# Performance work log

Measured on AMD Instinct MI355X. Metric: run time of the kernel, lower is better.

The kernel has to match this reference:

```python
import jax, jax.numpy as jnp
import numpy as np

N = 20000        # nodes
E = 320000       # edges (avg degree 16)
NHID = 256       # hidden dim (decoder input features)
NFEAT = 256      # reconstructed attribute dim
K_SELECTED = 4096  # number of nodes with label == 1 (static for jit)


def setup_inputs() -> dict:
    key = jax.random.key(0)
    ks = jax.random.split(key, 12)
    feature_attribute = jax.random.normal(ks[0], (N, NHID), dtype=jnp.float32)
    edge_row = jax.random.randint(ks[1], (E,), 0, N, dtype=jnp.int32)
    edge_col = jax.random.randint(ks[2], (E,), 0, N, dtype=jnp.int32)
    # positive, roughly degree-normalized adjacency weights
    edge_w = jax.random.uniform(ks[3], (E,), dtype=jnp.float32) / 16.0
    # first K_SELECTED nodes are labeled 1, rest 0 (static count for jit)
    labels = jnp.concatenate([jnp.ones((K_SELECTED,), jnp.int32),
                              jnp.zeros((N - K_SELECTED,), jnp.int32)])
    stdv1 = 1.0 / np.sqrt(NHID)
    stdv2 = 1.0 / np.sqrt(NFEAT)
    W1_ad = jax.random.uniform(ks[4], (NHID, NHID), minval=-stdv1, maxval=stdv1, dtype=jnp.float32)
    b1_ad = jax.random.uniform(ks[5], (NHID,), minval=-stdv1, maxval=stdv1, dtype=jnp.float32)
    W2_ad = jax.random.uniform(ks[6], (NHID, NFEAT), minval=-stdv2, maxval=stdv2, dtype=jnp.float32)
    b2_ad = jax.random.uniform(ks[7], (NFEAT,), minval=-stdv2, maxval=stdv2, dtype=jnp.float32)
    W_sd = jax.random.uniform(ks[8], (NHID, NHID), minval=-stdv1, maxval=stdv1, dtype=jnp.float32)
    b_sd = jax.random.uniform(ks[9], (NHID,), minval=-stdv1, maxval=stdv1, dtype=jnp.float32)
    return dict(feature_attribute=feature_attribute, edge_row=edge_row, edge_col=edge_col,
                edge_w=edge_w, labels=labels, W1_ad=W1_ad, b1_ad=b1_ad,
                W2_ad=W2_ad, b2_ad=b2_ad, W_sd=W_sd, b_sd=b_sd)


def reference(feature_attribute, edge_row, edge_col, edge_w, labels,
              W1_ad, b1_ad, W2_ad, b2_ad, W_sd, b_sd):
    def gcn(x, W, b):
        support = x @ W                                   # [N, d_out] dense mm
        msg = support[edge_col] * edge_w[:, None]         # gather + scale [E, d_out]
        out = jax.ops.segment_sum(msg, edge_row, num_segments=N)  # spmm aggregation
        return out + b

    # static-size index of labeled nodes (labels==1 count is K_SELECTED)
    idx = jnp.nonzero(labels == 1, size=K_SELECTED)[0]

    # Attribute decoder: relu(gc1) -> (dropout, eval: identity) -> gc2 -> select
    h = jax.nn.relu(gcn(feature_attribute, W1_ad, b1_ad))
    pred_attribute_mat = gcn(h, W2_ad, b2_ad)[idx]        # [K, NFEAT]

    # Structure decoder: gc1 -> select -> x @ x.T
    s = gcn(feature_attribute, W_sd, b_sd)[idx]           # [K, NHID]
    pred_adj_mat = s @ s.T                                # [K, K]

    return pred_attribute_mat, pred_adj_mat
```

## Files before the change

kernel.cpp:

```cpp
#include <hip/hip_runtime.h>
#include <hip/hip_bf16.h>

#define NN   20000
#define NE   320000
#define KSEL 4096

typedef short bf16x8 __attribute__((ext_vector_type(8)));
typedef float f32x4  __attribute__((ext_vector_type(4)));

static __device__ __forceinline__ float bf2f(unsigned short u){
  return __uint_as_float(((unsigned int)u) << 16);
}
static __device__ __forceinline__ unsigned short f2bf(float f){
  unsigned int x = __float_as_uint(f);
  x += 0x7fffu + ((x >> 16) & 1u);
  return (unsigned short)(x >> 16);
}
static __device__ __forceinline__ void gld_lds16(const unsigned short* g, unsigned short* l){
  __builtin_amdgcn_global_load_lds(
      (const __attribute__((address_space(1))) unsigned int*)g,
      (__attribute__((address_space(3))) unsigned int*)l, 16, 0, 0);
}

__global__ void k_cvt_x(const float* __restrict__ X, unsigned short* __restrict__ Xb){
  int i = (blockIdx.x * 256 + threadIdx.x) * 4;
  float4 v = *(const float4*)(X + i);
  ushort4 o = { f2bf(v.x), f2bf(v.y), f2bf(v.z), f2bf(v.w) };
  *(ushort4*)(Xb + i) = o;
}

__global__ void k_cvt_w(const float* __restrict__ W1, const float* __restrict__ Wsd,
                        const float* __restrict__ W2, unsigned short* __restrict__ Wt){
  int t = blockIdx.x * 256 + threadIdx.x;
  int w = t >> 16;
  int o = (t >> 8) & 255;
  int k = t & 255;
  const float* W = (w == 0) ? W1 : (w == 1 ? Wsd : W2);
  Wt[t] = f2bf(W[k * 256 + o]);
}

__global__ __launch_bounds__(256) void k_scan_part(const int* __restrict__ v, int n, int isLabel,
                                                   int* __restrict__ part){
  __shared__ int ws[4];
  int tid = threadIdx.x, lane = tid & 63, wv = tid >> 6;
  int base = blockIdx.x * 1024 + tid * 4;
  int s = 0;
  #pragma unroll
  for (int j = 0; j < 4; ++j){
    int n0 = base + j;
    if (n0 < n) s += isLabel ? (v[n0] == 1 ? 1 : 0) : v[n0];
  }
  #pragma unroll
  for (int off = 32; off; off >>= 1) s += __shfl_down(s, off, 64);
  if (lane == 0) ws[wv] = s;
  __syncthreads();
  if (tid == 0) part[blockIdx.x] = ws[0] + ws[1] + ws[2] + ws[3];
}

__global__ __launch_bounds__(64) void k_scan_offs(int* __restrict__ part, int P){
  int lane = threadIdx.x;
  int v = (lane < P) ? part[lane] : 0;
  int acc = v;
  #pragma unroll
  for (int off = 1; off < 64; off <<= 1){
    int t = __shfl_up(acc, off, 64);
    if (lane >= off) acc += t;
  }
  if (lane < P) part[lane] = acc - v;
}

__global__ __launch_bounds__(256) void k_idx_emit(const int* __restrict__ labels,
    const int* __restrict__ part, int* __restrict__ idx){
  __shared__ int ws[4];
  int tid = threadIdx.x, lane = tid & 63, wv = tid >> 6;
  int base = blockIdx.x * 1024 + tid * 4;
  int c[4]; int s = 0;
  #pragma unroll
  for (int j = 0; j < 4; ++j){
    int n0 = base + j;
    c[j] = (n0 < NN && labels[n0] == 1) ? 1 : 0;
    s += c[j];
  }
  int incl = s;
  #pragma unroll
  for (int off = 1; off < 64; off <<= 1){
    int t = __shfl_up(incl, off, 64);
    if (lane >= off) incl += t;
  }
  if (lane == 63) ws[wv] = incl;
  __syncthreads();
  int woff = part[blockIdx.x];
  for (int w = 0; w < wv; ++w) woff += ws[w];
  int off = woff + incl - s;
  #pragma unroll
  for (int j = 0; j < 4; ++j){
    if (c[j]){ if (off < KSEL) idx[off] = base + j; ++off; }
  }
}

__global__ __launch_bounds__(256) void k_row_emit(const int* __restrict__ counts,
    const int* __restrict__ part, int* __restrict__ start, int* __restrict__ cursor){
  __shared__ int ws[4];
  int tid = threadIdx.x, lane = tid & 63, wv = tid >> 6;
  int base = blockIdx.x * 1024 + tid * 4;
  int c[4]; int s = 0;
  #pragma unroll
  for (int j = 0; j < 4; ++j){
    int n0 = base + j;
    c[j] = (n0 < NN) ? counts[n0] : 0;
    s += c[j];
  }
  int incl = s;
  #pragma unroll
  for (int off = 1; off < 64; off <<= 1){
    int t = __shfl_up(incl, off, 64);
    if (lane >= off) incl += t;
  }
  if (lane == 63) ws[wv] = incl;
  __syncthreads();
  int woff = part[blockIdx.x];
  for (int w = 0; w < wv; ++w) woff += ws[w];
  int run = woff + incl - s;
  #pragma unroll
  for (int j = 0; j < 4; ++j){
    int n0 = base + j;
    if (n0 < NN){ start[n0] = run; cursor[n0] = run; run += c[j]; }
  }
  if (blockIdx.x == 0 && tid == 0) start[NN] = NE;
}

__global__ void k_hist(const int* __restrict__ row, int* __restrict__ counts){
  int e = blockIdx.x * 256 + threadIdx.x;
  if (e < NE) atomicAdd(&counts[row[e]], 1);
}

__global__ void k_scatter(const int* __restrict__ row, const int* __restrict__ col,
                          const float* __restrict__ ew, int* __restrict__ cursor,
                          int2* __restrict__ rec){
  int e = blockIdx.x * 256 + threadIdx.x;
  if (e < NE){
    int r = row[e];
    int p = atomicAdd(&cursor[r], 1);
    rec[p] = make_int2(col[e], __float_as_int(ew[e]));
  }
}

__global__ __launch_bounds__(256) void k_gemm(const unsigned short* __restrict__ A,
                                              const unsigned short* __restrict__ Wt,
                                              unsigned short* __restrict__ out,
                                              int M, int ldo){
  __shared__ unsigned short At[128 * 64];
  __shared__ unsigned short Bt[64 * 64];
  int tid = threadIdx.x, wave = tid >> 6, lane = tid & 63;
  int lm = lane & 15, lq = lane >> 4;
  int mBase = blockIdx.x * 128;
  int oBase = blockIdx.y * 64;
  f32x4 acc[2][4] = {};
  for (int kc = 0; kc < 256; kc += 64){
    if (kc) __syncthreads();
    #pragma unroll
    for (int it = 0; it < 4; ++it){
      int s = (wave * 4 + it) * 64 + lane;
      int row = s >> 3, c = (s & 7) ^ (row & 7);
      int gr = mBase + row; if (gr >= M) gr = M - 1;
      gld_lds16(&A[(size_t)gr * 256 + kc + c * 8], &At[s * 8]);
    }
    #pragma unroll
    for (int it = 0; it < 2; ++it){
      int s = (wave * 2 + it) * 64 + lane;
      int row = s >> 3, c = (s & 7) ^ (row & 7);
      gld_lds16(&Wt[(size_t)(oBase + row) * 256 + kc + c * 8], &Bt[s * 8]);
    }
    __syncthreads();
    #pragma unroll
    for (int ks = 0; ks < 64; ks += 32){
      int cb = ks >> 3;
      int RA = wave * 32 + lm;
      int ca = ((cb + lq) ^ (RA & 7)) << 3;
      bf16x8 a0 = *(const bf16x8*)&At[RA * 64 + ca];
      bf16x8 a1 = *(const bf16x8*)&At[(RA + 16) * 64 + ca];
      #pragma unroll
      for (int os = 0; os < 4; ++os){
        int RB = os * 16 + lm;
        bf16x8 b = *(const bf16x8*)&Bt[RB * 64 + (((cb + lq) ^ (RB & 7)) << 3)];
        acc[0][os] = __builtin_amdgcn_mfma_f32_16x16x32_bf16(a0, b, acc[0][os], 0, 0, 0);
        acc[1][os] = __builtin_amdgcn_mfma_f32_16x16x32_bf16(a1, b, acc[1][os], 0, 0, 0);
      }
    }
  }
  #pragma unroll
  for (int ms = 0; ms < 2; ++ms){
    int rb = mBase + wave * 32 + ms * 16 + lq * 4;
    #pragma unroll
    for (int os = 0; os < 4; ++os){
      int col = oBase + os * 16 + lm;
      #pragma unroll
      for (int r = 0; r < 4; ++r){
        int row = rb + r;
        if (row < M) out[(size_t)row * ldo + col] = f2bf(acc[ms][os][r]);
      }
    }
  }
}

__global__ __launch_bounds__(256) void k_gemm_out(const unsigned short* __restrict__ A,
                                                  const unsigned short* __restrict__ Wt2,
                                                  const float* __restrict__ bias,
                                                  float* __restrict__ out){
  __shared__ unsigned short lds[64 * 264];
  int tid = threadIdx.x;
  int wave = tid >> 6, lane = tid & 63;
  int lm = lane & 15, lq = lane >> 4;
  int mBase = blockIdx.x * 128;
  int oBase = blockIdx.y * 64;
  #pragma unroll
  for (int it = 0; it < 8; ++it){
    int c = it * 256 + tid;
    int o = c >> 5, kk = (c & 31) << 3;
    *(bf16x8*)&lds[o * 264 + kk] = *(const bf16x8*)&Wt2[(oBase + o) * 256 + kk];
  }
  __syncthreads();
  f32x4 acc[2][4] = {};
  int r0 = mBase + wave * 32 + lm;
  #pragma unroll
  for (int ks = 0; ks < 256; ks += 32){
    int ka = ks + lq * 8;
    bf16x8 a0 = *(const bf16x8*)&A[(size_t)r0 * 256 + ka];
    bf16x8 a1 = *(const bf16x8*)&A[(size_t)(r0 + 16) * 256 + ka];
    #pragma unroll
    for (int os = 0; os < 4; ++os){
      bf16x8 b = *(const bf16x8*)&lds[(os * 16 + lm) * 264 + ka];
      acc[0][os] = __builtin_amdgcn_mfma_f32_16x16x32_bf16(a0, b, acc[0][os], 0, 0, 0);
      acc[1][os] = __builtin_amdgcn_mfma_f32_16x16x32_bf16(a1, b, acc[1][os], 0, 0, 0);
    }
  }
  #pragma unroll
  for (int ms = 0; ms < 2; ++ms){
    int rb = mBase + wave * 32 + ms * 16 + lq * 4;
    #pragma unroll
    for (int os = 0; os < 4; ++os){
      int col = oBase + os * 16 + lm;
      float bv = bias[col];
      #pragma unroll
      for (int r = 0; r < 4; ++r)
        out[(size_t)(rb + r) * 256 + col] = acc[ms][os][r] + bv;
    }
  }
}

__global__ __launch_bounds__(256) void k_gemm_st(const unsigned short* __restrict__ S,
                                                 float* __restrict__ out1){
  __shared__ unsigned short At[128 * 64];
  __shared__ unsigned short Bt[128 * 64];
  int tid = threadIdx.x, wave = tid >> 6, lane = tid & 63;
  int lm = lane & 15, lq = lane >> 4;
  int mBase = blockIdx.x * 128;
  int oBase = blockIdx.y * 128;
  f32x4 acc[2][8] = {};
  for (int kc = 0; kc < 256; kc += 64){
    if (kc) __syncthreads();
    #pragma unroll
    for (int it = 0; it < 4; ++it){
      int s = (wave * 4 + it) * 64 + lane;
      int row = s >> 3, c = (s & 7) ^ (row & 7);
      gld_lds16(&S[(size_t)(mBase + row) * 256 + kc + c * 8], &At[s * 8]);
      gld_lds16(&S[(size_t)(oBase + row) * 256 + kc + c * 8], &Bt[s * 8]);
    }
    __syncthreads();
    #pragma unroll
    for (int ks = 0; ks < 64; ks += 32){
      int cb = ks >> 3;
      int RA = wave * 32 + lm;
      int ca = ((cb + lq) ^ (RA & 7)) << 3;
      bf16x8 a0 = *(const bf16x8*)&At[RA * 64 + ca];
      bf16x8 a1 = *(const bf16x8*)&At[(RA + 16) * 64 + ca];
      #pragma unroll
      for (int os = 0; os < 8; ++os){
        int RB = os * 16 + lm;
        bf16x8 b = *(const bf16x8*)&Bt[RB * 64 + (((cb + lq) ^ (RB & 7)) << 3)];
        acc[0][os] = __builtin_amdgcn_mfma_f32_16x16x32_bf16(a0, b, acc[0][os], 0, 0, 0);
        acc[1][os] = __builtin_amdgcn_mfma_f32_16x16x32_bf16(a1, b, acc[1][os], 0, 0, 0);
      }
    }
  }
  #pragma unroll
  for (int ms = 0; ms < 2; ++ms){
    int rb = mBase + wave * 32 + ms * 16 + lq * 4;
    #pragma unroll
    for (int os = 0; os < 8; ++os){
      int col = oBase + os * 16 + lm;
      #pragma unroll
      for (int r = 0; r < 4; ++r)
        out1[(size_t)(rb + r) * 4096 + col] = acc[ms][os][r];
    }
  }
}

__global__ __launch_bounds__(256) void k_spmm1(const unsigned short* __restrict__ supX,
    const int* __restrict__ start, const int2* __restrict__ rec,
    const float* __restrict__ b1, unsigned short* __restrict__ h){
  int wave = threadIdx.x >> 6, lane = threadIdx.x & 63;
  int n = blockIdx.x * 4 + wave;
  int s = start[n], e = start[n + 1];
  int d = lane * 4;
  float a0 = 0, a1 = 0, a2 = 0, a3 = 0;
  for (int base = s; base < e; base += 64){
    int p = base + lane;
    int pc = p < e ? p : e - 1;
    int2 r = rec[pc];
    float wv = (p < e) ? __int_as_float(r.y) : 0.0f;
    int m = e - base; if (m > 64) m = 64;
    for (int j = 0; j < m; j += 4){
      int   c0 = __shfl(r.x, j),     c1 = __shfl(r.x, j + 1);
      int   c2 = __shfl(r.x, j + 2), c3 = __shfl(r.x, j + 3);
      float w0 = __shfl(wv, j),      w1 = __shfl(wv, j + 1);
      float w2 = __shfl(wv, j + 2),  w3 = __shfl(wv, j + 3);
      ushort4 v0 = *(const ushort4*)&supX[(size_t)c0 * 512 + d];
      ushort4 v1 = *(const ushort4*)&supX[(size_t)c1 * 512 + d];
      ushort4 v2 = *(const ushort4*)&supX[(size_t)c2 * 512 + d];
      ushort4 v3 = *(const ushort4*)&supX[(size_t)c3 * 512 + d];
      a0 += w0 * bf2f(v0.x) + w1 * bf2f(v1.x) + w2 * bf2f(v2.x) + w3 * bf2f(v3.x);
      a1 += w0 * bf2f(v0.y) + w1 * bf2f(v1.y) + w2 * bf2f(v2.y) + w3 * bf2f(v3.y);
      a2 += w0 * bf2f(v0.z) + w1 * bf2f(v1.z) + w2 * bf2f(v2.z) + w3 * bf2f(v3.z);
      a3 += w0 * bf2f(v0.w) + w1 * bf2f(v1.w) + w2 * bf2f(v2.w) + w3 * bf2f(v3.w);
    }
  }
  float4 b = *(const float4*)&b1[d];
  ushort4 o = { f2bf(fmaxf(a0 + b.x, 0.f)), f2bf(fmaxf(a1 + b.y, 0.f)),
                f2bf(fmaxf(a2 + b.z, 0.f)), f2bf(fmaxf(a3 + b.w, 0.f)) };
  *(ushort4*)&h[(size_t)n * 256 + d] = o;
}

__global__ __launch_bounds__(256) void k_spmm_sel(const unsigned short* __restrict__ supX,
    const unsigned short* __restrict__ h, const int* __restrict__ idx,
    const int* __restrict__ start, const int2* __restrict__ rec,
    const float* __restrict__ bsd,
    unsigned short* __restrict__ aggH, unsigned short* __restrict__ sel){
  int wave = threadIdx.x >> 6, lane = threadIdx.x & 63;
  int i = blockIdx.x * 4 + wave;
  int n = idx[i];
  int s = start[n], e = start[n + 1];
  int d = lane * 4;
  float h0 = 0, h1 = 0, h2 = 0, h3 = 0;
  float s0 = 0, s1 = 0, s2 = 0, s3 = 0;
  for (int base = s; base < e; base += 64){
    int p = base + lane;
    int pc = p < e ? p : e - 1;
    int2 r = rec[pc];
    float wv = (p < e) ? __int_as_float(r.y) : 0.0f;
    int m = e - base; if (m > 64) m = 64;
    for (int j = 0; j < m; j += 2){
      int   c0 = __shfl(r.x, j), c1 = __shfl(r.x, j + 1);
      float w0 = __shfl(wv, j),  w1 = __shfl(wv, j + 1);
      ushort4 hv0 = *(const ushort4*)&h[(size_t)c0 * 256 + d];
      ushort4 sv0 = *(const ushort4*)&supX[(size_t)c0 * 512 + 256 + d];
      ushort4 hv1 = *(const ushort4*)&h[(size_t)c1 * 256 + d];
      ushort4 sv1 = *(const ushort4*)&supX[(size_t)c1 * 512 + 256 + d];
      h0 += w0 * bf2f(hv0.x) + w1 * bf2f(hv1.x);
      h1 += w0 * bf2f(hv0.y) + w1 * bf2f(hv1.y);
      h2 += w0 * bf2f(hv0.z) + w1 * bf2f(hv1.z);
      h3 += w0 * bf2f(hv0.w) + w1 * bf2f(hv1.w);
      s0 += w0 * bf2f(sv0.x) + w1 * bf2f(sv1.x);
      s1 += w0 * bf2f(sv0.y) + w1 * bf2f(sv1.y);
      s2 += w0 * bf2f(sv0.z) + w1 * bf2f(sv1.z);
      s3 += w0 * bf2f(sv0.w) + w1 * bf2f(sv1.w);
    }
  }
  ushort4 oh = { f2bf(h0), f2bf(h1), f2bf(h2), f2bf(h3) };
  *(ushort4*)&aggH[(size_t)i * 256 + d] = oh;
  float4 b = *(const float4*)&bsd[d];
  ushort4 os_ = { f2bf(s0 + b.x), f2bf(s1 + b.y), f2bf(s2 + b.z), f2bf(s3 + b.w) };
  *(ushort4*)&sel[(size_t)i * 256 + d] = os_;
}

extern "C" void kernel_launch(void* const* d_in, const int* in_sizes, int n_in,
                              void* d_out, int out_size, void* d_ws, size_t ws_size,
                              hipStream_t stream){
  const float* X    = (const float*)d_in[0];
  const int*   erow = (const int*)d_in[1];
  const int*   ecol = (const int*)d_in[2];
  const float* ew   = (const float*)d_in[3];
  const int*   labels = (const int*)d_in[4];
  const float* W1   = (const float*)d_in[5];
  const float* b1   = (const float*)d_in[6];
  const float* W2   = (const float*)d_in[7];
  const float* b2   = (const float*)d_in[8];
  const float* Wsd  = (const float*)d_in[9];
  const float* bsd  = (const float*)d_in[10];
  float* out0 = (float*)d_out;
  float* out1 = out0 + (size_t)KSEL * 256;

  char* ws = (char*)d_ws;
  unsigned short* Xb   = (unsigned short*)(ws);
  unsigned short* Wt   = (unsigned short*)(ws + 10240000);
  unsigned short* supX = (unsigned short*)(ws + 10633216);
  unsigned short* h    = (unsigned short*)(ws + 31113216);
  unsigned short* aggH = (unsigned short*)(ws + 41353216);
  unsigned short* sel  = (unsigned short*)(ws + 43450368);
  int* idx    = (int*)(ws + 45547520);
  int* counts = (int*)(ws + 45563904);
  int* startp = (int*)(ws + 45643904);
  int* cursor = (int*)(ws + 45723908);
  int2* rec   = (int2*)(ws + 45803912);
  int* partA  = (int*)(ws + 48363912);
  int* partB  = (int*)(ws + 48364040);

  hipMemsetAsync(counts, 0, NN * sizeof(int), stream);
  k_cvt_x<<<5000, 256, 0, stream>>>(X, Xb);
  k_cvt_w<<<768, 256, 0, stream>>>(W1, Wsd, W2, Wt);
  k_scan_part<<<20, 256, 0, stream>>>(labels, NN, 1, partA);
  k_scan_offs<<<1, 64, 0, stream>>>(partA, 20);
  k_idx_emit<<<20, 256, 0, stream>>>(labels, partA, idx);
  k_hist<<<NE / 256, 256, 0, stream>>>(erow, counts);
  k_scan_part<<<20, 256, 0, stream>>>(counts, NN, 0, partB);
  k_scan_offs<<<1, 64, 0, stream>>>(partB, 20);
  k_row_emit<<<20, 256, 0, stream>>>(counts, partB, startp, cursor);
  k_scatter<<<NE / 256, 256, 0, stream>>>(erow, ecol, ew, cursor, rec);
  k_gemm<<<dim3(157, 8), 256, 0, stream>>>(Xb, Wt, supX, NN, 512);
  k_spmm1<<<5000, 256, 0, stream>>>(supX, startp, rec, b1, h);
  k_spmm_sel<<<1024, 256, 0, stream>>>(supX, h, idx, startp, rec, bsd, aggH, sel);
  k_gemm_out<<<dim3(32, 4), 256, 0, stream>>>(aggH, Wt + 512 * 256, b2, out0);
  k_gemm_st<<<dim3(32, 32), 256, 0, stream>>>(sel, out1);
}
```

Measured before the change: 224.7 us.

## Aggregate before projecting and fuse prep kernels to cut GEMM and launches

Uses associativity (A·X)·W = A·(X·W) to run the sparse aggregation once on the raw features, shared by both first-layer GCNs. The full first-layer GEMM now covers only the W1 projection, and the structure decoder projects just the selected rows. The conversion, count-zeroing and label partial sums are merged into one prep kernel, and the separate scan-offset kernels are folded into the emit kernels, which removes several launches and the memset. The catch is that the row-emit blocks each re-sum the prefix of counts redundantly, and bf16 rounding now happens at a different point than before.

```diff
diff --git a/kernel.cpp b/kernel.cpp
--- a/kernel.cpp
+++ b/kernel.cpp
@@ -22,57 +22,61 @@
       (__attribute__((address_space(3))) unsigned int*)l, 16, 0, 0);
 }
 
-__global__ void k_cvt_x(const float* __restrict__ X, unsigned short* __restrict__ Xb){
-  int i = (blockIdx.x * 256 + threadIdx.x) * 4;
-  float4 v = *(const float4*)(X + i);
-  ushort4 o = { f2bf(v.x), f2bf(v.y), f2bf(v.z), f2bf(v.w) };
-  *(ushort4*)(Xb + i) = o;
-}
-
-__global__ void k_cvt_w(const float* __restrict__ W1, const float* __restrict__ Wsd,
-                        const float* __restrict__ W2, unsigned short* __restrict__ Wt){
-  int t = blockIdx.x * 256 + threadIdx.x;
-  int w = t >> 16;
-  int o = (t >> 8) & 255;
-  int k = t & 255;
-  const float* W = (w == 0) ? W1 : (w == 1 ? Wsd : W2);
-  Wt[t] = f2bf(W[k * 256 + o]);
-}
-
-__global__ __launch_bounds__(256) void k_scan_part(const int* __restrict__ v, int n, int isLabel,
-                                                   int* __restrict__ part){
+__global__ __launch_bounds__(256) void k_prep(const float* __restrict__ X,
+    const float* __restrict__ W1, const float* __restrict__ Wsd, const float* __restrict__ W2,
+    const int* __restrict__ labels,
+    unsigned short* __restrict__ Xb, unsigned short* __restrict__ Wt,
+    int* __restrict__ counts, int* __restrict__ partA){
+  int b = blockIdx.x, tid = threadIdx.x;
+  if (b < 5000){
+    int i = (b * 256 + tid) * 4;
+    float4 v = *(const float4*)(X + i);
+    ushort4 o = { f2bf(v.x), f2bf(v.y), f2bf(v.z), f2bf(v.w) };
+    *(ushort4*)(Xb + i) = o;
+  } else if (b < 5768){
+    int t = (b - 5000) * 256 + tid;
+    int w = t >> 16, o = (t >> 8) & 255, k = t & 255;
+    const float* W = (w == 0) ? W1 : (w == 1 ? Wsd : W2);
+    Wt[t] = f2bf(W[k * 256 + o]);
+  } else {
+    __shared__ int ws[4];
+    int z = b - 5768, lane = tid & 63, wv = tid >> 6;
+    if (tid < 250) *(int4*)&counts[z * 1000 + tid * 4] = make_int4(0, 0, 0, 0);
+    int base = z * 1024 + tid * 4;
+    int s = 0;
+    #pragma unroll
+    for (int j = 0; j < 4; ++j){
+      int n0 = base + j;
+      if (n0 < NN) s += (labels[n0] == 1) ? 1 : 0;
+    }
+    #pragma unroll
+    for (int off = 32; off; off >>= 1) s += __shfl_down(s, off, 64);
+    if (lane == 0) ws[wv] = s;
+    __syncthreads();
+    if (tid == 0) partA[z] = ws[0] + ws[1] + ws[2] + ws[3];
+  }
+}
+
+__global__ void k_hist(const int* __restrict__ row, int* __restrict__ counts){
+  int e = blockIdx.x * 256 + threadIdx.x;
+  if (e < NE) atomicAdd(&counts[row[e]], 1);
+}
+
+__global__ __launch_bounds__(256) void k_idx_emit(const int* __restrict__ labels,
+    const int* __restrict__ partA, int* __restrict__ idx){
   __shared__ int ws[4];
+  __shared__ int boff_s;
   int tid = threadIdx.x, lane = tid & 63, wv = tid >> 6;
-  int base = blockIdx.x * 1024 + tid * 4;
-  int s = 0;
-  #pragma unroll
-  for (int j = 0; j < 4; ++j){
-    int n0 = base + j;
-    if (n0 < n) s += isLabel ? (v[n0] == 1 ? 1 : 0) : v[n0];
-  }
-  #pragma unroll
-  for (int off = 32; off; off >>= 1) s += __shfl_down(s, off, 64);
-  if (lane == 0) ws[wv] = s;
-  __syncthreads();
-  if (tid == 0) part[blockIdx.x] = ws[0] + ws[1] + ws[2] + ws[3];
-}
-
-__global__ __launch_bounds__(64) void k_scan_offs(int* __restrict__ part, int P){
-  int lane = threadIdx.x;
-  int v = (lane < P) ? part[lane] : 0;
-  int acc = v;
-  #pragma unroll
-  for (int off = 1; off < 64; off <<= 1){
-    int t = __shfl_up(acc, off, 64);
-    if (lane >= off) acc += t;
-  }
-  if (lane < P) part[lane] = acc - v;
-}
-
-__global__ __launch_bounds__(256) void k_idx_emit(const int* __restrict__ labels,
-    const int* __restrict__ part, int* __restrict__ idx){
-  __shared__ int ws[4];
-  int tid = threadIdx.x, lane = tid & 63, wv = tid >> 6;
+  if (tid < 64){
+    int v = (lane < 20) ? partA[lane] : 0;
+    int acc = v;
+    #pragma unroll
+    for (int off = 1; off < 32; off <<= 1){
+      int t = __shfl_up(acc, off, 64);
+      if (lane >= off) acc += t;
+    }
+    if (lane == (int)blockIdx.x) boff_s = acc - v;
+  }
   int base = blockIdx.x * 1024 + tid * 4;
   int c[4]; int s = 0;
   #pragma unroll
@@ -89,7 +93,7 @@
   }
   if (lane == 63) ws[wv] = incl;
   __syncthreads();
-  int woff = part[blockIdx.x];
+  int woff = boff_s;
   for (int w = 0; w < wv; ++w) woff += ws[w];
   int off = woff + incl - s;
   #pragma unroll
@@ -99,14 +103,26 @@
 }
 
 __global__ __launch_bounds__(256) void k_row_emit(const int* __restrict__ counts,
-    const int* __restrict__ part, int* __restrict__ start, int* __restrict__ cursor){
+    int* __restrict__ start, int* __restrict__ cursor){
   __shared__ int ws[4];
+  __shared__ int red[4];
   int tid = threadIdx.x, lane = tid & 63, wv = tid >> 6;
-  int base = blockIdx.x * 1024 + tid * 4;
+  int base = blockIdx.x * 1024;
+  int ps = 0;
+  for (int i = tid * 4; i < base; i += 1024){
+    int4 v = *(const int4*)&counts[i];
+    ps += v.x + v.y + v.z + v.w;
+  }
+  #pragma unroll
+  for (int off = 32; off; off >>= 1) ps += __shfl_down(ps, off, 64);
+  if (lane == 0) red[wv] = ps;
+  __syncthreads();
+  int bpref = red[0] + red[1] + red[2] + red[3];
+  int nb = base + tid * 4;
   int c[4]; int s = 0;
   #pragma unroll
   for (int j = 0; j < 4; ++j){
-    int n0 = base + j;
+    int n0 = nb + j;
     c[j] = (n0 < NN) ? counts[n0] : 0;
     s += c[j];
   }
@@ -118,20 +134,15 @@
   }
   if (lane == 63) ws[wv] = incl;
   __syncthreads();
-  int woff = part[blockIdx.x];
+  int woff = bpref;
   for (int w = 0; w < wv; ++w) woff += ws[w];
   int run = woff + incl - s;
   #pragma unroll
   for (int j = 0; j < 4; ++j){
-    int n0 = base + j;
+    int n0 = nb + j;
     if (n0 < NN){ start[n0] = run; cursor[n0] = run; run += c[j]; }
   }
   if (blockIdx.x == 0 && tid == 0) start[NN] = NE;
-}
-
-__global__ void k_hist(const int* __restrict__ row, int* __restrict__ counts){
-  int e = blockIdx.x * 256 + threadIdx.x;
-  if (e < NE) atomicAdd(&counts[row[e]], 1);
 }
 
 __global__ void k_scatter(const int* __restrict__ row, const int* __restrict__ col,
@@ -145,160 +156,9 @@
   }
 }
 
-__global__ __launch_bounds__(256) void k_gemm(const unsigned short* __restrict__ A,
-                                              const unsigned short* __restrict__ Wt,
-                                              unsigned short* __restrict__ out,
-                                              int M, int ldo){
-  __shared__ unsigned short At[128 * 64];
-  __shared__ unsigned short Bt[64 * 64];
-  int tid = threadIdx.x, wave = tid >> 6, lane = tid & 63;
-  int lm = lane & 15, lq = lane >> 4;
-  int mBase = blockIdx.x * 128;
-  int oBase = blockIdx.y * 64;
-  f32x4 acc[2][4] = {};
-  for (int kc = 0; kc < 256; kc += 64){
-    if (kc) __syncthreads();
-    #pragma unroll
-    for (int it = 0; it < 4; ++it){
-      int s = (wave * 4 + it) * 64 + lane;
-      int row = s >> 3, c = (s & 7) ^ (row & 7);
-      int gr = mBase + row; if (gr >= M) gr = M - 1;
-      gld_lds16(&A[(size_t)gr * 256 + kc + c * 8], &At[s * 8]);
-    }
-    #pragma unroll
-    for (int it = 0; it < 2; ++it){
-      int s = (wave * 2 + it) * 64 + lane;
-      int row = s >> 3, c = (s & 7) ^ (row & 7);
-      gld_lds16(&Wt[(size_t)(oBase + row) * 256 + kc + c * 8], &Bt[s * 8]);
-    }
-    __syncthreads();
-    #pragma unroll
-    for (int ks = 0; ks < 64; ks += 32){
-      int cb = ks >> 3;
-      int RA = wave * 32 + lm;
-      int ca = ((cb + lq) ^ (RA & 7)) << 3;
-      bf16x8 a0 = *(const bf16x8*)&At[RA * 64 + ca];
-      bf16x8 a1 = *(const bf16x8*)&At[(RA + 16) * 64 + ca];
-      #pragma unroll
-      for (int os = 0; os < 4; ++os){
-        int RB = os * 16 + lm;
-        bf16x8 b = *(const bf16x8*)&Bt[RB * 64 + (((cb + lq) ^ (RB & 7)) << 3)];
-        acc[0][os] = __builtin_amdgcn_mfma_f32_16x16x32_bf16(a0, b, acc[0][os], 0, 0, 0);
-        acc[1][os] = __builtin_amdgcn_mfma_f32_16x16x32_bf16(a1, b, acc[1][os], 0, 0, 0);
-      }
-    }
-  }
-  #pragma unroll
-  for (int ms = 0; ms < 2; ++ms){
-    int rb = mBase + wave * 32 + ms * 16 + lq * 4;
-    #pragma unroll
-    for (int os = 0; os < 4; ++os){
-      int col = oBase + os * 16 + lm;
-      #pragma unroll
-      for (int r = 0; r < 4; ++r){
-        int row = rb + r;
-        if (row < M) out[(size_t)row * ldo + col] = f2bf(acc[ms][os][r]);
-      }
-    }
-  }
-}
-
-__global__ __launch_bounds__(256) void k_gemm_out(const unsigned short* __restrict__ A,
-                                                  const unsigned short* __restrict__ Wt2,
-                                                  const float* __restrict__ bias,
-                                                  float* __restrict__ out){
-  __shared__ unsigned short lds[64 * 264];
-  int tid = threadIdx.x;
-  int wave = tid >> 6, lane = tid & 63;
-  int lm = lane & 15, lq = lane >> 4;
-  int mBase = blockIdx.x * 128;
-  int oBase = blockIdx.y * 64;
-  #pragma unroll
-  for (int it = 0; it < 8; ++it){
-    int c = it * 256 + tid;
-    int o = c >> 5, kk = (c & 31) << 3;
-    *(bf16x8*)&lds[o * 264 + kk] = *(const bf16x8*)&Wt2[(oBase + o) * 256 + kk];
-  }
-  __syncthreads();
-  f32x4 acc[2][4] = {};
-  int r0 = mBase + wave * 32 + lm;
-  #pragma unroll
-  for (int ks = 0; ks < 256; ks += 32){
-    int ka = ks + lq * 8;
-    bf16x8 a0 = *(const bf16x8*)&A[(size_t)r0 * 256 + ka];
-    bf16x8 a1 = *(const bf16x8*)&A[(size_t)(r0 + 16) * 256 + ka];
-    #pragma unroll
-    for (int os = 0; os < 4; ++os){
-      bf16x8 b = *(const bf16x8*)&lds[(os * 16 + lm) * 264 + ka];
-      acc[0][os] = __builtin_amdgcn_mfma_f32_16x16x32_bf16(a0, b, acc[0][os], 0, 0, 0);
-      acc[1][os] = __builtin_amdgcn_mfma_f32_16x16x32_bf16(a1, b, acc[1][os], 0, 0, 0);
-    }
-  }
-  #pragma unroll
-  for (int ms = 0; ms < 2; ++ms){
-    int rb = mBase + wave * 32 + ms * 16 + lq * 4;
-    #pragma unroll
-    for (int os = 0; os < 4; ++os){
-      int col = oBase + os * 16 + lm;
-      float bv = bias[col];
-      #pragma unroll
-      for (int r = 0; r < 4; ++r)
-        out[(size_t)(rb + r) * 256 + col] = acc[ms][os][r] + bv;
-    }
-  }
-}
-
-__global__ __launch_bounds__(256) void k_gemm_st(const unsigned short* __restrict__ S,
-                                                 float* __restrict__ out1){
-  __shared__ unsigned short At[128 * 64];
-  __shared__ unsigned short Bt[128 * 64];
-  int tid = threadIdx.x, wave = tid >> 6, lane = tid & 63;
-  int lm = lane & 15, lq = lane >> 4;
-  int mBase = blockIdx.x * 128;
-  int oBase = blockIdx.y * 128;
-  f32x4 acc[2][8] = {};
-  for (int kc = 0; kc < 256; kc += 64){
-    if (kc) __syncthreads();
-    #pragma unroll
-    for (int it = 0; it < 4; ++it){
-      int s = (wave * 4 + it) * 64 + lane;
-      int row = s >> 3, c = (s & 7) ^ (row & 7);
-      gld_lds16(&S[(size_t)(mBase + row) * 256 + kc + c * 8], &At[s * 8]);
-      gld_lds16(&S[(size_t)(oBase + row) * 256 + kc + c * 8], &Bt[s * 8]);
-    }
-    __syncthreads();
-    #pragma unroll
-    for (int ks = 0; ks < 64; ks += 32){
-      int cb = ks >> 3;
-      int RA = wave * 32 + lm;
-      int ca = ((cb + lq) ^ (RA & 7)) << 3;
-      bf16x8 a0 = *(const bf16x8*)&At[RA * 64 + ca];
-      bf16x8 a1 = *(const bf16x8*)&At[(RA + 16) * 64 + ca];
-      #pragma unroll
-      for (int os = 0; os < 8; ++os){
-        int RB = os * 16 + lm;
-        bf16x8 b = *(const bf16x8*)&Bt[RB * 64 + (((cb + lq) ^ (RB & 7)) << 3)];
-        acc[0][os] = __builtin_amdgcn_mfma_f32_16x16x32_bf16(a0, b, acc[0][os], 0, 0, 0);
-        acc[1][os] = __builtin_amdgcn_mfma_f32_16x16x32_bf16(a1, b, acc[1][os], 0, 0, 0);
-      }
-    }
-  }
-  #pragma unroll
-  for (int ms = 0; ms < 2; ++ms){
-    int rb = mBase + wave * 32 + ms * 16 + lq * 4;
-    #pragma unroll
-    for (int os = 0; os < 8; ++os){
-      int col = oBase + os * 16 + lm;
-      #pragma unroll
-      for (int r = 0; r < 4; ++r)
-        out1[(size_t)(rb + r) * 4096 + col] = acc[ms][os][r];
-    }
-  }
-}
-
-__global__ __launch_bounds__(256) void k_spmm1(const unsigned short* __restrict__ supX,
+__global__ __launch_bounds__(256) void k_spmm_full(const unsigned short* __restrict__ Xb,
     const int* __restrict__ start, const int2* __restrict__ rec,
-    const float* __restrict__ b1, unsigned short* __restrict__ h){
+    unsigned short* __restrict__ aggX){
   int wave = threadIdx.x >> 6, lane = threadIdx.x & 63;
   int n = blockIdx.x * 4 + wave;
   int s = start[n], e = start[n + 1];
@@ -315,62 +175,220 @@
       int   c2 = __shfl(r.x, j + 2), c3 = __shfl(r.x, j + 3);
       float w0 = __shfl(wv, j),      w1 = __shfl(wv, j + 1);
       float w2 = __shfl(wv, j + 2),  w3 = __shfl(wv, j + 3);
-      ushort4 v0 = *(const ushort4*)&supX[(size_t)c0 * 512 + d];
-      ushort4 v1 = *(const ushort4*)&supX[(size_t)c1 * 512 + d];
-      ushort4 v2 = *(const ushort4*)&supX[(size_t)c2 * 512 + d];
-      ushort4 v3 = *(const ushort4*)&supX[(size_t)c3 * 512 + d];
+      ushort4 v0 = *(const ushort4*)&Xb[(size_t)c0 * 256 + d];
+      ushort4 v1 = *(const ushort4*)&Xb[(size_t)c1 * 256 + d];
+      ushort4 v2 = *(const ushort4*)&Xb[(size_t)c2 * 256 + d];
+      ushort4 v3 = *(const ushort4*)&Xb[(size_t)c3 * 256 + d];
       a0 += w0 * bf2f(v0.x) + w1 * bf2f(v1.x) + w2 * bf2f(v2.x) + w3 * bf2f(v3.x);
       a1 += w0 * bf2f(v0.y) + w1 * bf2f(v1.y) + w2 * bf2f(v2.y) + w3 * bf2f(v3.y);
       a2 += w0 * bf2f(v0.z) + w1 * bf2f(v1.z) + w2 * bf2f(v2.z) + w3 * bf2f(v3.z);
       a3 += w0 * bf2f(v0.w) + w1 * bf2f(v1.w) + w2 * bf2f(v2.w) + w3 * bf2f(v3.w);
     }
   }
-  float4 b = *(const float4*)&b1[d];
-  ushort4 o = { f2bf(fmaxf(a0 + b.x, 0.f)), f2bf(fmaxf(a1 + b.y, 0.f)),
-                f2bf(fmaxf(a2 + b.z, 0.f)), f2bf(fmaxf(a3 + b.w, 0.f)) };
-  *(ushort4*)&h[(size_t)n * 256 + d] = o;
-}
-
-__global__ __launch_bounds__(256) void k_spmm_sel(const unsigned short* __restrict__ supX,
-    const unsigned short* __restrict__ h, const int* __restrict__ idx,
-    const int* __restrict__ start, const int2* __restrict__ rec,
-    const float* __restrict__ bsd,
-    unsigned short* __restrict__ aggH, unsigned short* __restrict__ sel){
+  ushort4 o = { f2bf(a0), f2bf(a1), f2bf(a2), f2bf(a3) };
+  *(ushort4*)&aggX[(size_t)n * 256 + d] = o;
+}
+
+__global__ __launch_bounds__(256) void k_gemm_h(const unsigned short* __restrict__ A,
+                                                const unsigned short* __restrict__ Wt,
+                                                const float* __restrict__ bias,
+                                                unsigned short* __restrict__ out, int M){
+  __shared__ unsigned short At[128 * 64];
+  __shared__ unsigned short Bt[64 * 64];
+  int tid = threadIdx.x, wave = tid >> 6, lane = tid & 63;
+  int lm = lane & 15, lq = lane >> 4;
+  int mBase = blockIdx.x * 128;
+  int oBase = blockIdx.y * 64;
+  f32x4 acc[2][4] = {};
+  for (int kc = 0; kc < 256; kc += 64){
+    if (kc) __syncthreads();
+    #pragma unroll
+    for (int it = 0; it < 4; ++it){
+      int s = (wave * 4 + it) * 64 + lane;
+      int row = s >> 3, c = (s & 7) ^ (row & 7);
+      int gr = mBase + row; if (gr >= M) gr = M - 1;
+      gld_lds16(&A[(size_t)gr * 256 + kc + c * 8], &At[s * 8]);
+    }
+    #pragma unroll
+    for (int it = 0; it < 2; ++it){
+      int s = (wave * 2 + it) * 64 + lane;
+      int row = s >> 3, c = (s & 7) ^ (row & 7);
+      gld_lds16(&Wt[(size_t)(oBase + row) * 256 + kc + c * 8], &Bt[s * 8]);
+    }
+    __syncthreads();
+    #pragma unroll
+    for (int ks = 0; ks < 64; ks += 32){
+      int cb = ks >> 3;
+      int RA = wave * 32 + lm;
+      int ca = ((cb + lq) ^ (RA & 7)) << 3;
+      bf16x8 a0 = *(const bf16x8*)&At[RA * 64 + ca];
+      bf16x8 a1 = *(const bf16x8*)&At[(RA + 16) * 64 + ca];
+      #pragma unroll
+      for (int os = 0; os < 4; ++os){
+        int RB = os * 16 + lm;
+        bf16x8 b = *(const bf16x8*)&Bt[RB * 64 + (((cb + lq) ^ (RB & 7)) << 3)];
+        acc[0][os] = __builtin_amdgcn_mfma_f32_16x16x32_bf16(a0, b, acc[0][os], 0, 0, 0);
+        acc[1][os] = __builtin_amdgcn_mfma_f32_16x16x32_bf16(a1, b, acc[1][os], 0, 0, 0);
+      }
+    }
+  }
+  #pragma unroll
+  for (int ms = 0; ms < 2; ++ms){
+    int rb = mBase + wave * 32 + ms * 16 + lq * 4;
+    #pragma unroll
+    for (int os = 0; os < 4; ++os){
+      int col = oBase + os * 16 + lm;
+      float bv = bias[col];
+      #pragma unroll
+      for (int r = 0; r < 4; ++r){
+        int row = rb + r;
+        if (row < M) out[(size_t)row * 256 + col] = f2bf(fmaxf(acc[ms][os][r] + bv, 0.f));
+      }
+    }
+  }
+}
+
+__global__ __launch_bounds__(256) void k_spmm_selH(const unsigned short* __restrict__ h,
+    const int* __restrict__ idx, const int* __restrict__ start, const int2* __restrict__ rec,
+    unsigned short* __restrict__ aggH){
   int wave = threadIdx.x >> 6, lane = threadIdx.x & 63;
   int i = blockIdx.x * 4 + wave;
   int n = idx[i];
   int s = start[n], e = start[n + 1];
   int d = lane * 4;
-  float h0 = 0, h1 = 0, h2 = 0, h3 = 0;
-  float s0 = 0, s1 = 0, s2 = 0, s3 = 0;
+  float a0 = 0, a1 = 0, a2 = 0, a3 = 0;
   for (int base = s; base < e; base += 64){
     int p = base + lane;
     int pc = p < e ? p : e - 1;
     int2 r = rec[pc];
     float wv = (p < e) ? __int_as_float(r.y) : 0.0f;
     int m = e - base; if (m > 64) m = 64;
-    for (int j = 0; j < m; j += 2){
-      int   c0 = __shfl(r.x, j), c1 = __shfl(r.x, j + 1);
-      float w0 = __shfl(wv, j),  w1 = __shfl(wv, j + 1);
-      ushort4 hv0 = *(const ushort4*)&h[(size_t)c0 * 256 + d];
-      ushort4 sv0 = *(const ushort4*)&supX[(size_t)c0 * 512 + 256 + d];
-      ushort4 hv1 = *(const ushort4*)&h[(size_t)c1 * 256 + d];
-      ushort4 sv1 = *(const ushort4*)&supX[(size_t)c1 * 512 + 256 + d];
-      h0 += w0 * bf2f(hv0.x) + w1 * bf2f(hv1.x);
-      h1 += w0 * bf2f(hv0.y) + w1 * bf2f(hv1.y);
-      h2 += w0 * bf2f(hv0.z) + w1 * bf2f(hv1.z);
-      h3 += w0 * bf2f(hv0.w) + w1 * bf2f(hv1.w);
-      s0 += w0 * bf2f(sv0.x) + w1 * bf2f(sv1.x);
-      s1 += w0 * bf2f(sv0.y) + w1 * bf2f(sv1.y);
-      s2 += w0 * bf2f(sv0.z) + w1 * bf2f(sv1.z);
-      s3 += w0 * bf2f(sv0.w) + w1 * bf2f(sv1.w);
-    }
-  }
-  ushort4 oh = { f2bf(h0), f2bf(h1), f2bf(h2), f2bf(h3) };
-  *(ushort4*)&aggH[(size_t)i * 256 + d] = oh;
-  float4 b = *(const float4*)&bsd[d];
-  ushort4 os_ = { f2bf(s0 + b.x), f2bf(s1 + b.y), f2bf(s2 + b.z), f2bf(s3 + b.w) };
-  *(ushort4*)&sel[(size_t)i * 256 + d] = os_;
+    for (int j = 0; j < m; j += 4){
+      int   c0 = __shfl(r.x, j),     c1 = __shfl(r.x, j + 1);
+      int   c2 = __shfl(r.x, j + 2), c3 = __shfl(r.x, j + 3);
+      float w0 = __shfl(wv, j),      w1 = __shfl(wv, j + 1);
+      float w2 = __shfl(wv, j + 2),  w3 = __shfl(wv, j + 3);
+      ushort4 v0 = *(const ushort4*)&h[(size_t)c0 * 256 + d];
+      ushort4 v1 = *(const ushort4*)&h[(size_t)c1 * 256 + d];
+      ushort4 v2 = *(const ushort4*)&h[(size_t)c2 * 256 + d];
+      ushort4 v3 = *(const ushort4*)&h[(size_t)c3 * 256 + d];
+      a0 += w0 * bf2f(v0.x) + w1 * bf2f(v1.x) + w2 * bf2f(v2.x) + w3 * bf2f(v3.x);
+      a1 += w0 * bf2f(v0.y) + w1 * bf2f(v1.y) + w2 * bf2f(v2.y) + w3 * bf2f(v3.y);
+      a2 += w0 * bf2f(v0.z) + w1 * bf2f(v1.z) + w2 * bf2f(v2.z) + w3 * bf2f(v3.z);
+      a3 += w0 * bf2f(v0.w) + w1 * bf2f(v1.w) + w2 * bf2f(v2.w) + w3 * bf2f(v3.w);
+    }
+  }
+  ushort4 o = { f2bf(a0), f2bf(a1), f2bf(a2), f2bf(a3) };
+  *(ushort4*)&aggH[(size_t)i * 256 + d] = o;
+}
+
+__global__ __launch_bounds__(256) void k_gemm_os(const unsigned short* __restrict__ aggH,
+    const unsigned short* __restrict__ aggX, const int* __restrict__ idx,
+    const unsigned short* __restrict__ Wt,
+    const float* __restrict__ b2, const float* __restrict__ bsd,
+    float* __restrict__ out0, unsigned short* __restrict__ sel){
+  __shared__ unsigned short lds[64 * 264];
+  int tid = threadIdx.x;
+  int wave = tid >> 6, lane = tid & 63;
+  int lm = lane & 15, lq = lane >> 4;
+  int z = blockIdx.z;
+  int mBase = blockIdx.x * 128;
+  int oBase = blockIdx.y * 64;
+  const unsigned short* Wt2 = Wt + (z ? 256 * 256 : 512 * 256);
+  const float* bias = z ? bsd : b2;
+  #pragma unroll
+  for (int it = 0; it < 8; ++it){
+    int c = it * 256 + tid;
+    int o = c >> 5, kk = (c & 31) << 3;
+    *(bf16x8*)&lds[o * 264 + kk] = *(const bf16x8*)&Wt2[(oBase + o) * 256 + kk];
+  }
+  __syncthreads();
+  int r0 = mBase + wave * 32 + lm;
+  const unsigned short* A0;
+  const unsigned short* A1;
+  if (z){
+    A0 = aggX + (size_t)idx[r0] * 256;
+    A1 = aggX + (size_t)idx[r0 + 16] * 256;
+  } else {
+    A0 = aggH + (size_t)r0 * 256;
+    A1 = aggH + (size_t)(r0 + 16) * 256;
+  }
+  f32x4 acc[2][4] = {};
+  #pragma unroll
+  for (int ks = 0; ks < 256; ks += 32){
+    int ka = ks + lq * 8;
+    bf16x8 a0 = *(const bf16x8*)&A0[ka];
+    bf16x8 a1 = *(const bf16x8*)&A1[ka];
+    #pragma unroll
+    for (int os = 0; os < 4; ++os){
+      bf16x8 b = *(const bf16x8*)&lds[(os * 16 + lm) * 264 + ka];
+      acc[0][os] = __builtin_amdgcn_mfma_f32_16x16x32_bf16(a0, b, acc[0][os], 0, 0, 0);
+      acc[1][os] = __builtin_amdgcn_mfma_f32_16x16x32_bf16(a1, b, acc[1][os], 0, 0, 0);
+    }
+  }
+  #pragma unroll
+  for (int ms = 0; ms < 2; ++ms){
+    int rb = mBase + wave * 32 + ms * 16 + lq * 4;
+    #pragma unroll
+    for (int os = 0; os < 4; ++os){
+      int col = oBase + os * 16 + lm;
+      float bv = bias[col];
+      #pragma unroll
+      for (int r = 0; r < 4; ++r){
+        float v = acc[ms][os][r] + bv;
+        if (z) sel[(size_t)(rb + r) * 256 + col] = f2bf(v);
+        else   out0[(size_t)(rb + r) * 256 + col] = v;
+      }
+    }
+  }
+}
+
+__global__ __launch_bounds__(256) void k_gemm_st(const unsigned short* __restrict__ S,
+                                                 float* __restrict__ out1){
+  __shared__ unsigned short At[128 * 64];
+  __shared__ unsigned short Bt[128 * 64];
+  int tid = threadIdx.x, wave = tid >> 6, lane = tid & 63;
+  int lm = lane & 15, lq = lane >> 4;
+  int mBase = blockIdx.x * 128;
+  int oBase = blockIdx.y * 128;
+  f32x4 acc[2][8] = {};
+  for (int kc = 0; kc < 256; kc += 64){
+    if (kc) __syncthreads();
+    #pragma unroll
+    for (int it = 0; it < 4; ++it){
+      int s = (wave * 4 + it) * 64 + lane;
+      int row = s >> 3, c = (s & 7) ^ (row & 7);
+      gld_lds16(&S[(size_t)(mBase + row) * 256 + kc + c * 8], &At[s * 8]);
+      gld_lds16(&S[(size_t)(oBase + row) * 256 + kc + c * 8], &Bt[s * 8]);
+    }
+    __syncthreads();
+    #pragma unroll
+    for (int ks = 0; ks < 64; ks += 32){
+      int cb = ks >> 3;
+      int RA = wave * 32 + lm;
+      int ca = ((cb + lq) ^ (RA & 7)) << 3;
+      bf16x8 a0 = *(const bf16x8*)&At[RA * 64 + ca];
+      bf16x8 a1 = *(const bf16x8*)&At[(RA + 16) * 64 + ca];
+      #pragma unroll
+      for (int os = 0; os < 8; ++os){
+        int RB = os * 16 + lm;
+        bf16x8 b = *(const bf16x8*)&Bt[RB * 64 + (((cb + lq) ^ (RB & 7)) << 3)];
+        acc[0][os] = __builtin_amdgcn_mfma_f32_16x16x32_bf16(a0, b, acc[0][os], 0, 0, 0);
+        acc[1][os] = __builtin_amdgcn_mfma_f32_16x16x32_bf16(a1, b, acc[1][os], 0, 0, 0);
+      }
+    }
+  }
+  #pragma unroll
+  for (int ms = 0; ms < 2; ++ms){
+    int rb = mBase + wave * 32 + ms * 16 + lq * 4;
+    #pragma unroll
+    for (int os = 0; os < 8; ++os){
+      int col = oBase + os * 16 + lm;
+      #pragma unroll
+      for (int r = 0; r < 4; ++r)
+        out1[(size_t)(rb + r) * 4096 + col] = acc[ms][os][r];
+    }
+  }
 }
 
 extern "C" void kernel_launch(void* const* d_in, const int* in_sizes, int n_in,
@@ -393,32 +411,25 @@
   char* ws = (char*)d_ws;
   unsigned short* Xb   = (unsigned short*)(ws);
   unsigned short* Wt   = (unsigned short*)(ws + 10240000);
-  unsigned short* supX = (unsigned short*)(ws + 10633216);
-  unsigned short* h    = (unsigned short*)(ws + 31113216);
-  unsigned short* aggH = (unsigned short*)(ws + 41353216);
-  unsigned short* sel  = (unsigned short*)(ws + 43450368);
-  int* idx    = (int*)(ws + 45547520);
-  int* counts = (int*)(ws + 45563904);
-  int* startp = (int*)(ws + 45643904);
-  int* cursor = (int*)(ws + 45723908);
-  int2* rec   = (int2*)(ws + 45803912);
-  int* partA  = (int*)(ws + 48363912);
-  int* partB  = (int*)(ws + 48364040);
-
-  hipMemsetAsync(counts, 0, NN * sizeof(int), stream);
-  k_cvt_x<<<5000, 256, 0, stream>>>(X, Xb);
-  k_cvt_w<<<768, 256, 0, stream>>>(W1, Wsd, W2, Wt);
-  k_scan_part<<<20, 256, 0, stream>>>(labels, NN, 1, partA);
-  k_scan_offs<<<1, 64, 0, stream>>>(partA, 20);
+  unsigned short* aggX = (unsigned short*)(ws + 10633216);
+  unsigned short* h    = (unsigned short*)(ws + 20873216);
+  unsigned short* aggH = (unsigned short*)(ws + 31113216);
+  unsigned short* sel  = (unsigned short*)(ws + 33210368);
+  int* idx    = (int*)(ws + 35307520);
+  int* counts = (int*)(ws + 35323904);
+  int* startp = (int*)(ws + 35403904);
+  int* cursor = (int*)(ws + 35483908);
+  int2* rec   = (int2*)(ws + 35563912);
+  int* partA  = (int*)(ws + 38123912);
+
+  k_prep<<<5788, 256, 0, stream>>>(X, W1, Wsd, W2, labels, Xb, Wt, counts, partA);
+  k_hist<<<NE / 256, 256, 0, stream>>>(erow, counts);
   k_idx_emit<<<20, 256, 0, stream>>>(labels, partA, idx);
-  k_hist<<<NE / 256, 256, 0, stream>>>(erow, counts);
-  k_scan_part<<<20, 256, 0, stream>>>(counts, NN, 0, partB);
-  k_scan_offs<<<1, 64, 0, stream>>>(partB, 20);
-  k_row_emit<<<20, 256, 0, stream>>>(counts, partB, startp, cursor);
+  k_row_emit<<<20, 256, 0, stream>>>(counts, startp, cursor);
   k_scatter<<<NE / 256, 256, 0, stream>>>(erow, ecol, ew, cursor, rec);
-  k_gemm<<<dim3(157, 8), 256, 0, stream>>>(Xb, Wt, supX, NN, 512);
-  k_spmm1<<<5000, 256, 0, stream>>>(supX, startp, rec, b1, h);
-  k_spmm_sel<<<1024, 256, 0, stream>>>(supX, h, idx, startp, rec, bsd, aggH, sel);
-  k_gemm_out<<<dim3(32, 4), 256, 0, stream>>>(aggH, Wt + 512 * 256, b2, out0);
+  k_spmm_full<<<5000, 256, 0, stream>>>(Xb, startp, rec, aggX);
+  k_gemm_h<<<dim3(157, 4), 256, 0, stream>>>(aggX, Wt, b1, h, NN);
+  k_spmm_selH<<<1024, 256, 0, stream>>>(h, idx, startp, rec, aggH);
+  k_gemm_os<<<dim3(32, 4, 2), 256, 0, stream>>>(aggH, aggX, idx, Wt, b2, bsd, out0, sel);
   k_gemm_st<<<dim3(32, 32), 256, 0, stream>>>(sel, out1);
 }
```

Result: faster. 208.1 us (-7.4%).
